# Kernel optimization log

Hardware: AMD Instinct MI355X
Metric: run time of the kernel (lower is better)

## Reference

```python
import jax, jax.numpy as jnp
import numpy as np

PARALLEL = 4
EPS = 1e-5

# Binarization with sign (straight-through estimator in bwd; fwd is just sign)
@jax.custom_vjp
def binarize(x):
    return jnp.sign(x)

def _bin_fwd(x):
    return jnp.sign(x), x

def _bin_bwd(x, g):
    return (g * (jnp.abs(x) <= 1.0).astype(g.dtype),)

binarize.defvjp(_bin_fwd, _bin_bwd)


def bconv3x3(x, w, groups, stride=1):
    # XNOR-style conv: binarize activations and weights, grouped 3x3, pad 1
    return jax.lax.conv_general_dilated(
        binarize(x), binarize(w),
        window_strides=(stride, stride),
        padding=[(1, 1), (1, 1)],
        feature_group_count=groups,
        dimension_numbers=('NCHW', 'OIHW', 'NCHW'))


def batchnorm(x, scale, bias, mean, var):
    inv = scale * jax.lax.rsqrt(var + EPS)
    return x * inv[None, :, None, None] + (bias - mean * inv)[None, :, None, None]


def setup_inputs() -> dict:
    key = jax.random.key(0)
    ks = jax.random.split(key, 12)
    f32 = jnp.float32
    return {
        'x':         jax.random.normal(ks[0], (32, 256, 28, 28), dtype=f32),
        'w1':        jax.random.normal(ks[1], (1024, 256, 3, 3), dtype=f32),
        'bn1_scale': jax.random.uniform(ks[2], (1024,), dtype=f32),
        'bn1_bias':  jax.random.normal(ks[3], (1024,), dtype=f32),
        'bn1_mean':  jax.random.normal(ks[4], (1024,), dtype=f32),
        'bn1_var':   jax.random.uniform(ks[5], (1024,), dtype=f32),
        'w2':        jax.random.normal(ks[6], (1024, 256, 3, 3), dtype=f32),
        'bn2_scale': jax.random.uniform(ks[7], (1024,), dtype=f32),
        'bn2_bias':  jax.random.normal(ks[8], (1024,), dtype=f32),
        'bn2_mean':  jax.random.normal(ks[9], (1024,), dtype=f32),
        'bn2_var':   jax.random.uniform(ks[10], (1024,), dtype=f32),
        'lambdas':   jax.random.uniform(ks[11], (4,), dtype=f32),
    }


def reference(x, w1, bn1_scale, bn1_bias, bn1_mean, bn1_var,
              w2, bn2_scale, bn2_bias, bn2_mean, bn2_var, lambdas):
    identity = x  # downsample is None
    # squeeze: repeat channels parallel times -> [B, 1024, H, W]
    xr = jnp.tile(x, (1, PARALLEL, 1, 1))
    out = bconv3x3(xr, w1, groups=PARALLEL, stride=1)
    out = jax.nn.relu(batchnorm(out, bn1_scale, bn1_bias, bn1_mean, bn1_var))
    out = bconv3x3(out, w2, groups=PARALLEL, stride=1)
    out = batchnorm(out, bn2_scale, bn2_bias, bn2_mean, bn2_var)
    B, C, H, W = out.shape
    planes = C // PARALLEL
    # multiplication: per-group scalar lambda, broadcast over planes within each group
    out = out * jnp.repeat(lambdas, planes)[None, :, None, None]
    # squeeze: sum over parallel groups -> [B, planes, H, W]
    out = out.reshape(B, PARALLEL, planes, H, W).sum(axis=1)
    return jax.nn.relu(out + identity)
```

## Files before the change

kernel.cpp:

```cpp
#include <hip/hip_runtime.h>
#include <cstdint>

#define BN_EPS 1e-5f

typedef unsigned int uint;
typedef int v4i __attribute__((ext_vector_type(4)));
typedef int v16i __attribute__((ext_vector_type(16)));
typedef short v4h __attribute__((ext_vector_type(4)));


#define RSTR 7680
#define TILE6 46080

__global__ __launch_bounds__(256) void kPrep(
    const float* __restrict__ s1, const float* __restrict__ b1,
    const float* __restrict__ m1, const float* __restrict__ v1,
    const float* __restrict__ s2, const float* __restrict__ b2,
    const float* __restrict__ m2, const float* __restrict__ v2,
    const float* __restrict__ lam,
    float* __restrict__ thr1, float* __restrict__ bnA2,
    float* __restrict__ bbSum) {
  int t = blockIdx.x * 256 + threadIdx.x;
  if (t >= 1024) return;
  float inv1 = s1[t] / sqrtf(v1[t] + BN_EPS);
  float bb1 = b1[t] - m1[t] * inv1;
  thr1[t] = -bb1 / inv1;
  float inv2 = s2[t] / sqrtf(v2[t] + BN_EPS);
  bnA2[t] = inv2 * lam[t >> 8];
  if (t < 256) {
    float s = 0.f;
#pragma unroll
    for (int g = 0; g < 4; g++) {
      int i = g * 256 + t;
      float iv = s2[i] / sqrtf(v2[i] + BN_EPS);
      s += (b2[i] - m2[i] * iv) * lam[g];
    }
    bbSum[t] = s;
  }
}

__global__ __launch_bounds__(256) void kQ1(const float* __restrict__ x,
                                           char* __restrict__ A1i) {
  const int tid = threadIdx.x;
  const int lane = tid & 63, cb = tid >> 6;
  const int grp = blockIdx.x;
  const int b = grp / 49, p0 = (grp % 49) * 16;
  __shared__ char t[16][256];
  const float4* src =
      (const float4*)(x + ((size_t)(b * 256 + cb * 64 + lane) * 784 + p0));
  float4 f0 = src[0], f1 = src[1], f2 = src[2], f3 = src[3];
  const int c = cb * 64 + lane;
#define Q(V, J) t[J][c] = ((V) >= 0.f) ? (char)1 : (char)-1;
  Q(f0.x, 0)  Q(f0.y, 1)  Q(f0.z, 2)  Q(f0.w, 3)
  Q(f1.x, 4)  Q(f1.y, 5)  Q(f1.z, 6)  Q(f1.w, 7)
  Q(f2.x, 8)  Q(f2.y, 9)  Q(f2.z, 10) Q(f2.w, 11)
  Q(f3.x, 12) Q(f3.y, 13) Q(f3.z, 14) Q(f3.w, 15)
#undef Q
  __syncthreads();
  const int px = tid >> 4, ch = tid & 15;
  *(v4i*)(A1i + (size_t)(b * 784 + p0 + px) * 256 + ch * 16) =
      *(const v4i*)(&t[px][ch * 16]);
}

__global__ __launch_bounds__(256) void kWf(const float* __restrict__ w,
                                           char* __restrict__ Wf) {
  const int oc = blockIdx.x, ic = threadIdx.x;
  const float* s = w + (size_t)(oc * 256 + ic) * 9;
  const int ocb = oc >> 5;
  const int l = (oc & 31) + ((ic >> 4) & 1) * 32;
  const int kk = ic >> 5, j = ic & 15;
  char* base = Wf + (size_t)(ocb * 72 + kk) * 1024 + l * 16 + j;
#pragma unroll
  for (int tap = 0; tap < 9; tap++)
    base[(size_t)tap * 8 * 1024] = (s[tap] >= 0.f) ? (char)1 : (char)-1;
}

__global__ __launch_bounds__(256) void kConv1M(
    const char* __restrict__ A1i, const char* __restrict__ Wf1,
    const float* __restrict__ thr1, char* __restrict__ A2i) {
  const int tid = threadIdx.x;
  const int l = tid & 63, w = tid >> 6;
  const int xg = blockIdx.x;
  const int xcd = xg & 7, s = xg >> 3;
  const int ocq = xcd >> 1;
  const int b = (s / 7) * 2 + (xcd & 1);
  const int yt = s % 7;
  const int y0 = yt * 4;

  __shared__ char tile[TILE6];
  __shared__ float thrT[256];

  for (int i = tid; i < TILE6 / 16; i += 256) ((v4i*)tile)[i] = (v4i){0,0,0,0};
  thrT[tid] = thr1[ocq * 256 + tid];
  __syncthreads();
  {
    const char* src = A1i + (size_t)b * 784 * 256;
    for (int i = tid; i < 2688; i += 256) {
      int r = i / 448, jj = i - r * 448;
      int px = jj >> 4, ch = jj & 15;
      int ry = y0 - 1 + r;
      if (ry >= 0 && ry < 28) {
        v4i v = *(const v4i*)(src + (size_t)(ry * 28 + px) * 256 + ch * 16);
        int cl = px + 1;
        *(v4i*)(tile + r * RSTR + cl * 256 + ((ch * 16) ^ ((cl & 15) << 4))) = v;
      }
    }
  }
  __syncthreads();

  const int col = l & 31, krow = l >> 5;
  int cbase[4], xm[4][3];
#pragma unroll
  for (int nb = 0; nb < 4; nb++) {
    int px = nb * 32 + col;
    int pxc = (px < 112) ? px : 111;
    int yy = pxc / 28, xx = pxc - yy * 28;
    cbase[nb] = yy * RSTR + xx * 256 + krow * 16;
#pragma unroll
    for (int e = 0; e < 3; e++) xm[nb][e] = ((xx + e) & 15) << 4;
  }

  v16i acc[2][4];
#pragma unroll
  for (int na = 0; na < 2; na++)
#pragma unroll
    for (int nb = 0; nb < 4; nb++) acc[na][nb] = (v16i)(0);
  const char* wb = Wf1 + (size_t)(ocq * 8 + w * 2) * 73728 + l * 16;

  for (int d = 0; d < 3; d++) {
#pragma unroll
    for (int e = 0; e < 3; e++) {
      const char* wp = wb + (size_t)(d * 3 + e) * 8192;
#pragma unroll
      for (int kk = 0; kk < 8; kk++) {
        v4i a0 = *(const v4i*)(wp + kk * 1024);
        v4i a1 = *(const v4i*)(wp + 73728 + kk * 1024);
#pragma unroll
        for (int nb = 0; nb < 4; nb++) {
          int baddr = cbase[nb] + d * RSTR + e * 256 + kk * 32;
          v4i bf = *(const v4i*)(tile + (baddr ^ xm[nb][e]));
          acc[0][nb] = __builtin_amdgcn_mfma_i32_32x32x32_i8(a0, bf, acc[0][nb], 0, 0, 0);
          acc[1][nb] = __builtin_amdgcn_mfma_i32_32x32x32_i8(a1, bf, acc[1][nb], 0, 0, 0);
        }
      }
    }
  }

  __syncthreads();
  char* bt = tile;
#pragma unroll
  for (int na = 0; na < 2; na++) {
#pragma unroll
    for (int nb = 0; nb < 4; nb++) {
      int px = nb * 32 + col;
      if (px < 112) {
#pragma unroll
        for (int qg = 0; qg < 4; qg++) {
          int ocb4 = w * 64 + na * 32 + qg * 8 + 4 * krow;
          float4 th = *(const float4*)&thrT[ocb4];
          uint word = 0;
          word |= ((float)acc[na][nb][qg * 4 + 0] > th.x) ? 0x01u : 0u;
          word |= ((float)acc[na][nb][qg * 4 + 1] > th.y) ? 0x100u : 0u;
          word |= ((float)acc[na][nb][qg * 4 + 2] > th.z) ? 0x10000u : 0u;
          word |= ((float)acc[na][nb][qg * 4 + 3] > th.w) ? 0x1000000u : 0u;
          *(uint*)(bt + px * 256 + (ocb4 ^ ((px & 15) << 4))) = word;
        }
      }
    }
  }
  __syncthreads();
  {
    char* dst = A2i + (size_t)(b * 784 + y0 * 28) * 1024 + ocq * 256;
    for (int i = tid; i < 1792; i += 256) {
      int p2 = i >> 4, ch = i & 15;
      v4i v = *(const v4i*)(bt + p2 * 256 + ((ch * 16) ^ ((p2 & 15) << 4)));
      *(v4i*)(dst + (size_t)p2 * 1024 + ch * 16) = v;
    }
  }
}

__global__ __launch_bounds__(256) void kConv2P(
    const char* __restrict__ A2i, const char* __restrict__ Wf2,
    short* __restrict__ P16, int b0, int NBc) {
  const int tid = threadIdx.x;
  const int l = tid & 63, w = tid >> 6;
  const int xg = blockIdx.x;
  const int xcd = xg & 7, s = xg >> 3;
  const int g = xcd >> 1;
  const int bl = (s / 7) * 2 + (xcd & 1);
  const int yt = s % 7;
  const int b = b0 + bl;
  const int y0 = yt * 4;

  __shared__ char tile[TILE6];

  for (int i = tid; i < TILE6 / 16; i += 256) ((v4i*)tile)[i] = (v4i){0,0,0,0};
  __syncthreads();
  {
    const char* src = A2i + (size_t)b * 784 * 1024 + g * 256;
    for (int i = tid; i < 2688; i += 256) {
      int r = i / 448, jj = i - r * 448;
      int px = jj >> 4, ch = jj & 15;
      int ry = y0 - 1 + r;
      if (ry >= 0 && ry < 28) {
        v4i v = *(const v4i*)(src + (size_t)(ry * 28 + px) * 1024 + ch * 16);
        int cl = px + 1;
        *(v4i*)(tile + r * RSTR + cl * 256 + ((ch * 16) ^ ((cl & 15) << 4))) = v;
      }
    }
  }
  __syncthreads();

  const int col = l & 31, krow = l >> 5;
  int cbase[4], xm[4][3];
#pragma unroll
  for (int nb = 0; nb < 4; nb++) {
    int px = nb * 32 + col;
    int pxc = (px < 112) ? px : 111;
    int yy = pxc / 28, xx = pxc - yy * 28;
    cbase[nb] = yy * RSTR + xx * 256 + krow * 16;
#pragma unroll
    for (int e = 0; e < 3; e++) xm[nb][e] = ((xx + e) & 15) << 4;
  }

  v16i acc[2][4];
#pragma unroll
  for (int na = 0; na < 2; na++)
#pragma unroll
    for (int nb = 0; nb < 4; nb++) acc[na][nb] = (v16i)(0);
  const char* wb = Wf2 + (size_t)(g * 8 + w * 2) * 73728 + l * 16;

  for (int d = 0; d < 3; d++) {
#pragma unroll
    for (int e = 0; e < 3; e++) {
      const char* wp = wb + (size_t)(d * 3 + e) * 8192;
#pragma unroll
      for (int kk = 0; kk < 8; kk++) {
        v4i a0 = *(const v4i*)(wp + kk * 1024);
        v4i a1 = *(const v4i*)(wp + 73728 + kk * 1024);
#pragma unroll
        for (int nb = 0; nb < 4; nb++) {
          int baddr = cbase[nb] + d * RSTR + e * 256 + kk * 32;
          v4i bf = *(const v4i*)(tile + (baddr ^ xm[nb][e]));
          acc[0][nb] = __builtin_amdgcn_mfma_i32_32x32x32_i8(a0, bf, acc[0][nb], 0, 0, 0);
          acc[1][nb] = __builtin_amdgcn_mfma_i32_32x32x32_i8(a1, bf, acc[1][nb], 0, 0, 0);
        }
      }
    }
  }

  short* base = P16 + ((size_t)((g * NBc + bl) * 784) + y0 * 28) * 256;
#pragma unroll
  for (int na = 0; na < 2; na++) {
#pragma unroll
    for (int nb = 0; nb < 4; nb++) {
      int px = nb * 32 + col;
      if (px < 112) {
        short* pp = base + px * 256 + w * 64 + na * 32 + 4 * krow;
#pragma unroll
        for (int qg = 0; qg < 4; qg++) {
          v4h v = {(short)acc[na][nb][qg * 4 + 0], (short)acc[na][nb][qg * 4 + 1],
                   (short)acc[na][nb][qg * 4 + 2], (short)acc[na][nb][qg * 4 + 3]};
          *(v4h*)(pp + 8 * qg) = v;
        }
      }
    }
  }
}

__global__ __launch_bounds__(256) void kRed(
    const short* __restrict__ P16, const float* __restrict__ bnA2,
    const float* __restrict__ bbSum, const float* __restrict__ xin,
    float* __restrict__ out, int b0, int NBc) {
  const int tid = threadIdx.x;
  const int y = blockIdx.x, bl = blockIdx.y, b = b0 + bl;

  __shared__ float vals[256 * 29];

  float cf[4];
#pragma unroll
  for (int g = 0; g < 4; g++) cf[g] = bnA2[g * 256 + tid];
  const float bbs = bbSum[tid];
  const short* Pp[4];
#pragma unroll
  for (int g = 0; g < 4; g++)
    Pp[g] = P16 + ((size_t)((g * NBc + bl) * 784) + y * 28) * 256 + tid;

  for (int x = 0; x < 28; x++) {
    float v = bbs;
#pragma unroll
    for (int g = 0; g < 4; g++)
      v += cf[g] * (float)(int)Pp[g][x * 256];
    vals[tid * 29 + x] = v;
  }
  __syncthreads();

#pragma unroll
  for (int k = 0; k < 7; k++) {
    int f = tid + 256 * k;
    int c = f / 7, xq = f - 7 * c;
    size_t base = ((size_t)(b * 256 + c) * 28 + y) * 28 + xq * 4;
    float4 xi = *(const float4*)(xin + base);
    float4 o;
    o.x = fmaxf(vals[c * 29 + xq * 4 + 0] + xi.x, 0.0f);
    o.y = fmaxf(vals[c * 29 + xq * 4 + 1] + xi.y, 0.0f);
    o.z = fmaxf(vals[c * 29 + xq * 4 + 2] + xi.z, 0.0f);
    o.w = fmaxf(vals[c * 29 + xq * 4 + 3] + xi.w, 0.0f);
    *(float4*)(out + base) = o;
  }
}

extern "C" void kernel_launch(void* const* d_in, const int* in_sizes, int n_in,
                              void* d_out, int out_size, void* d_ws, size_t ws_size,
                              hipStream_t stream) {
  const float* x   = (const float*)d_in[0];
  const float* w1  = (const float*)d_in[1];
  const float* s1  = (const float*)d_in[2];
  const float* b1  = (const float*)d_in[3];
  const float* m1  = (const float*)d_in[4];
  const float* v1  = (const float*)d_in[5];
  const float* w2  = (const float*)d_in[6];
  const float* s2  = (const float*)d_in[7];
  const float* b2  = (const float*)d_in[8];
  const float* m2  = (const float*)d_in[9];
  const float* v2  = (const float*)d_in[10];
  const float* lam = (const float*)d_in[11];
  float* out = (float*)d_out;

  char* ws = (char*)d_ws;
  char*  A1i   = ws + 0;
  char*  Wf1   = ws + 6422528;
  char*  Wf2   = ws + 8781824;
  char*  A2i   = ws + 11141120;
  float* thr1  = (float*)(ws + 36831232);
  float* bnA2  = (float*)(ws + 36835328);
  float* bbSum = (float*)(ws + 36839424);
  short* P16   = (short*)(ws + 36843520);

  const size_t needFull = 36843520ull + 4ull * 32 * 784 * 256 * 2;
  const int NBc = (ws_size >= needFull) ? 32 : 16;

  kPrep<<<4, 256, 0, stream>>>(s1, b1, m1, v1, s2, b2, m2, v2, lam,
                               thr1, bnA2, bbSum);
  kQ1<<<1568, 256, 0, stream>>>(x, A1i);
  kWf<<<1024, 256, 0, stream>>>(w1, Wf1);
  kWf<<<1024, 256, 0, stream>>>(w2, Wf2);
  kConv1M<<<896, 256, 0, stream>>>(A1i, Wf1, thr1, A2i);
  for (int b0 = 0; b0 < 32; b0 += NBc) {
    kConv2P<<<8 * (NBc / 2) * 7, 256, 0, stream>>>(A2i, Wf2, P16, b0, NBc);
    kRed<<<dim3(28, NBc), 256, 0, stream>>>(P16, bnA2, bbSum, x, out, b0, NBc);
  }
}
```

Before: 230.8 us.

## Halve output-channel tile per block in both binary convs, doubling grid size

Each conv block now computes 128 output channels instead of 256, holding one accumulator set per wave rather than two, and the grid for both conv kernels doubles. This lowers register pressure and raises the number of blocks, which can improve occupancy and load balance across CUs. In exchange, each input tile is staged into shared memory twice as often, and every A-fragment load now feeds only four MFMAs instead of eight, so data reuse per load drops.

```diff
diff --git a/kernel.cpp b/kernel.cpp
--- a/kernel.cpp
+++ b/kernel.cpp
@@ -81,17 +81,15 @@
   const int tid = threadIdx.x;
   const int l = tid & 63, w = tid >> 6;
   const int xg = blockIdx.x;
-  const int xcd = xg & 7, s = xg >> 3;
-  const int ocq = xcd >> 1;
-  const int b = (s / 7) * 2 + (xcd & 1);
-  const int yt = s % 7;
+  const int ocH = xg & 7, s = xg >> 3;
+  const int b = s / 7, yt = s % 7;
   const int y0 = yt * 4;
 
   __shared__ char tile[TILE6];
-  __shared__ float thrT[256];
+  __shared__ float thrT[128];
 
   for (int i = tid; i < TILE6 / 16; i += 256) ((v4i*)tile)[i] = (v4i){0,0,0,0};
-  thrT[tid] = thr1[ocq * 256 + tid];
+  if (tid < 128) thrT[tid] = thr1[ocH * 128 + tid];
   __syncthreads();
   {
     const char* src = A1i + (size_t)b * 784 * 256;
@@ -120,12 +118,10 @@
     for (int e = 0; e < 3; e++) xm[nb][e] = ((xx + e) & 15) << 4;
   }
 
-  v16i acc[2][4];
-#pragma unroll
-  for (int na = 0; na < 2; na++)
-#pragma unroll
-    for (int nb = 0; nb < 4; nb++) acc[na][nb] = (v16i)(0);
-  const char* wb = Wf1 + (size_t)(ocq * 8 + w * 2) * 73728 + l * 16;
+  v16i acc[4];
+#pragma unroll
+  for (int nb = 0; nb < 4; nb++) acc[nb] = (v16i)(0);
+  const char* wb = Wf1 + (size_t)(ocH * 4 + w) * 73728 + l * 16;
 
   for (int d = 0; d < 3; d++) {
 #pragma unroll
@@ -134,13 +130,11 @@
 #pragma unroll
       for (int kk = 0; kk < 8; kk++) {
         v4i a0 = *(const v4i*)(wp + kk * 1024);
-        v4i a1 = *(const v4i*)(wp + 73728 + kk * 1024);
 #pragma unroll
         for (int nb = 0; nb < 4; nb++) {
           int baddr = cbase[nb] + d * RSTR + e * 256 + kk * 32;
           v4i bf = *(const v4i*)(tile + (baddr ^ xm[nb][e]));
-          acc[0][nb] = __builtin_amdgcn_mfma_i32_32x32x32_i8(a0, bf, acc[0][nb], 0, 0, 0);
-          acc[1][nb] = __builtin_amdgcn_mfma_i32_32x32x32_i8(a1, bf, acc[1][nb], 0, 0, 0);
+          acc[nb] = __builtin_amdgcn_mfma_i32_32x32x32_i8(a0, bf, acc[nb], 0, 0, 0);
         }
       }
     }
@@ -149,30 +143,27 @@
   __syncthreads();
   char* bt = tile;
 #pragma unroll
-  for (int na = 0; na < 2; na++) {
-#pragma unroll
-    for (int nb = 0; nb < 4; nb++) {
-      int px = nb * 32 + col;
-      if (px < 112) {
-#pragma unroll
-        for (int qg = 0; qg < 4; qg++) {
-          int ocb4 = w * 64 + na * 32 + qg * 8 + 4 * krow;
-          float4 th = *(const float4*)&thrT[ocb4];
-          uint word = 0;
-          word |= ((float)acc[na][nb][qg * 4 + 0] > th.x) ? 0x01u : 0u;
-          word |= ((float)acc[na][nb][qg * 4 + 1] > th.y) ? 0x100u : 0u;
-          word |= ((float)acc[na][nb][qg * 4 + 2] > th.z) ? 0x10000u : 0u;
-          word |= ((float)acc[na][nb][qg * 4 + 3] > th.w) ? 0x1000000u : 0u;
-          *(uint*)(bt + px * 256 + (ocb4 ^ ((px & 15) << 4))) = word;
-        }
+  for (int nb = 0; nb < 4; nb++) {
+    int px = nb * 32 + col;
+    if (px < 112) {
+#pragma unroll
+      for (int qg = 0; qg < 4; qg++) {
+        int ocb4 = w * 32 + qg * 8 + 4 * krow;
+        float4 th = *(const float4*)&thrT[ocb4];
+        uint word = 0;
+        word |= ((float)acc[nb][qg * 4 + 0] > th.x) ? 0x01u : 0u;
+        word |= ((float)acc[nb][qg * 4 + 1] > th.y) ? 0x100u : 0u;
+        word |= ((float)acc[nb][qg * 4 + 2] > th.z) ? 0x10000u : 0u;
+        word |= ((float)acc[nb][qg * 4 + 3] > th.w) ? 0x1000000u : 0u;
+        *(uint*)(bt + px * 256 + (ocb4 ^ ((px & 15) << 4))) = word;
       }
     }
   }
   __syncthreads();
   {
-    char* dst = A2i + (size_t)(b * 784 + y0 * 28) * 1024 + ocq * 256;
-    for (int i = tid; i < 1792; i += 256) {
-      int p2 = i >> 4, ch = i & 15;
+    char* dst = A2i + (size_t)(b * 784 + y0 * 28) * 1024 + ocH * 128;
+    for (int i = tid; i < 896; i += 256) {
+      int p2 = i >> 3, ch = i & 7;
       v4i v = *(const v4i*)(bt + p2 * 256 + ((ch * 16) ^ ((p2 & 15) << 4)));
       *(v4i*)(dst + (size_t)p2 * 1024 + ch * 16) = v;
     }
@@ -186,9 +177,8 @@
   const int l = tid & 63, w = tid >> 6;
   const int xg = blockIdx.x;
   const int xcd = xg & 7, s = xg >> 3;
-  const int g = xcd >> 1;
-  const int bl = (s / 7) * 2 + (xcd & 1);
-  const int yt = s % 7;
+  const int g = xcd >> 1, ocH = xcd & 1;
+  const int bl = s / 7, yt = s % 7;
   const int b = b0 + bl;
   const int y0 = yt * 4;
 
@@ -223,12 +213,10 @@
     for (int e = 0; e < 3; e++) xm[nb][e] = ((xx + e) & 15) << 4;
   }
 
-  v16i acc[2][4];
-#pragma unroll
-  for (int na = 0; na < 2; na++)
-#pragma unroll
-    for (int nb = 0; nb < 4; nb++) acc[na][nb] = (v16i)(0);
-  const char* wb = Wf2 + (size_t)(g * 8 + w * 2) * 73728 + l * 16;
+  v16i acc[4];
+#pragma unroll
+  for (int nb = 0; nb < 4; nb++) acc[nb] = (v16i)(0);
+  const char* wb = Wf2 + (size_t)(g * 8 + ocH * 4 + w) * 73728 + l * 16;
 
   for (int d = 0; d < 3; d++) {
 #pragma unroll
@@ -237,13 +225,11 @@
 #pragma unroll
       for (int kk = 0; kk < 8; kk++) {
         v4i a0 = *(const v4i*)(wp + kk * 1024);
-        v4i a1 = *(const v4i*)(wp + 73728 + kk * 1024);
 #pragma unroll
         for (int nb = 0; nb < 4; nb++) {
           int baddr = cbase[nb] + d * RSTR + e * 256 + kk * 32;
           v4i bf = *(const v4i*)(tile + (baddr ^ xm[nb][e]));
-          acc[0][nb] = __builtin_amdgcn_mfma_i32_32x32x32_i8(a0, bf, acc[0][nb], 0, 0, 0);
-          acc[1][nb] = __builtin_amdgcn_mfma_i32_32x32x32_i8(a1, bf, acc[1][nb], 0, 0, 0);
+          acc[nb] = __builtin_amdgcn_mfma_i32_32x32x32_i8(a0, bf, acc[nb], 0, 0, 0);
         }
       }
     }
@@ -251,18 +237,15 @@
 
   short* base = P16 + ((size_t)((g * NBc + bl) * 784) + y0 * 28) * 256;
 #pragma unroll
-  for (int na = 0; na < 2; na++) {
-#pragma unroll
-    for (int nb = 0; nb < 4; nb++) {
-      int px = nb * 32 + col;
-      if (px < 112) {
-        short* pp = base + px * 256 + w * 64 + na * 32 + 4 * krow;
-#pragma unroll
-        for (int qg = 0; qg < 4; qg++) {
-          v4h v = {(short)acc[na][nb][qg * 4 + 0], (short)acc[na][nb][qg * 4 + 1],
-                   (short)acc[na][nb][qg * 4 + 2], (short)acc[na][nb][qg * 4 + 3]};
-          *(v4h*)(pp + 8 * qg) = v;
-        }
+  for (int nb = 0; nb < 4; nb++) {
+    int px = nb * 32 + col;
+    if (px < 112) {
+      short* pp = base + px * 256 + ocH * 128 + w * 32 + 4 * krow;
+#pragma unroll
+      for (int qg = 0; qg < 4; qg++) {
+        v4h v = {(short)acc[nb][qg * 4 + 0], (short)acc[nb][qg * 4 + 1],
+                 (short)acc[nb][qg * 4 + 2], (short)acc[nb][qg * 4 + 3]};
+        *(v4h*)(pp + 8 * qg) = v;
       }
     }
   }
@@ -345,9 +328,9 @@
   kQ1<<<1568, 256, 0, stream>>>(x, A1i);
   kWf<<<1024, 256, 0, stream>>>(w1, Wf1);
   kWf<<<1024, 256, 0, stream>>>(w2, Wf2);
-  kConv1M<<<896, 256, 0, stream>>>(A1i, Wf1, thr1, A2i);
+  kConv1M<<<1792, 256, 0, stream>>>(A1i, Wf1, thr1, A2i);
   for (int b0 = 0; b0 < 32; b0 += NBc) {
-    kConv2P<<<8 * (NBc / 2) * 7, 256, 0, stream>>>(A2i, Wf2, P16, b0, NBc);
+    kConv2P<<<8 * NBc * 7, 256, 0, stream>>>(A2i, Wf2, P16, b0, NBc);
     kRed<<<dim3(28, NBc), 256, 0, stream>>>(P16, bnA2, bbSum, x, out, b0, NBc);
   }
 }
```

After: 227.6 us. Within noise of the previous version (-1.4%).
